# Optimization experiments

Measured on AMD Instinct MI355X. Metric: run time of the kernel, lower is better.

The kernel has to match this reference:

```python
import jax, jax.numpy as jnp
import numpy as np

EMBED_DIM = 2048
HIDDEN_DIM = 2048
SEQ_LEN = 8192


def setup_inputs() -> dict:
    key = jax.random.key(0)
    ks = jax.random.split(key, 6)
    x = jax.random.normal(ks[0], (SEQ_LEN, EMBED_DIM), dtype=jnp.float32)
    # original uses torch.rand (uniform [0,1)) for params
    W_h = jax.random.uniform(ks[1], (HIDDEN_DIM, HIDDEN_DIM), dtype=jnp.float32)
    W_x = jax.random.uniform(ks[2], (HIDDEN_DIM, EMBED_DIM), dtype=jnp.float32)
    W_y = jax.random.uniform(ks[3], (EMBED_DIM, HIDDEN_DIM), dtype=jnp.float32)
    B_h = jax.random.uniform(ks[4], (HIDDEN_DIM,), dtype=jnp.float32)
    B_y = jax.random.uniform(ks[5], (EMBED_DIM,), dtype=jnp.float32)
    return {"x": x, "W_h": W_h, "W_x": W_x, "W_y": W_y, "B_h": B_h, "B_y": B_y}


def reference(x, W_h, W_x, W_y, B_h, B_y):
    # Precompute input projections for all timesteps in one GEMM: [T, H]
    xp = x @ W_x.T + B_h

    def step(h, xp_t):
        h_new = jnp.tanh(W_h @ h + xp_t)  # [H]
        return h_new, h_new

    h0 = jnp.zeros((W_h.shape[0],), dtype=x.dtype)
    h_final, hs = jax.lax.scan(step, h0, xp)  # hs: [T, H]
    # Output projection + softmax over embed dim, batched over timesteps
    logits = hs @ W_y.T + B_y  # [T, E]
    output = jax.nn.softmax(logits, axis=-1)
    return (h_final, output)
```

## Files before the change

### kernel.cpp

```cpp
#include <hip/hip_runtime.h>

#define T_SEQ 8192
#define HDIM  2048
#define EDIM  2048
#define RBLK  64
#define ROWS_PER_BLK (HDIM / RBLK)

typedef unsigned long long u64;
typedef __attribute__((ext_vector_type(4))) unsigned int u32x4;
typedef __attribute__((ext_vector_type(4))) float f32x4;

__device__ inline void poll_pair(const u64* p0, const u64* p1, u32x4& a, u32x4& b) {
    asm volatile("global_load_dwordx4 %0, %2, off sc1\n\t"
                 "global_load_dwordx4 %1, %3, off sc1\n\t"
                 "s_waitcnt vmcnt(0)"
                 : "=v"(a), "=v"(b) : "v"(p0), "v"(p1) : "memory");
}

__device__ inline f32x4 ld_w16(const float* p) {
    f32x4 r;
    asm volatile("global_load_dwordx4 %0, %1, off" : "=v"(r) : "v"(p));
    return r;
}

__global__ __launch_bounds__(256) void gemm_nt_bias(
    const float* __restrict__ A, const float* __restrict__ B,
    const float* __restrict__ bias, float* __restrict__ C,
    int M, int N, int K)
{
    constexpr int BK = 32;
    __shared__ float As[BK][64 + 4];
    __shared__ float Bs[BK][64 + 4];

    const int tx = threadIdx.x & 15;
    const int ty = threadIdx.x >> 4;
    const int m0 = blockIdx.y * 64;
    const int n0 = blockIdx.x * 64;

    float acc[4][4] = {};

    for (int kk = 0; kk < K; kk += BK) {
        #pragma unroll
        for (int p = 0; p < 8; ++p) {
            int idx = p * 256 + threadIdx.x;
            int r = idx >> 5;
            int c = idx & 31;
            As[c][r] = A[(size_t)(m0 + r) * K + kk + c];
            Bs[c][r] = B[(size_t)(n0 + r) * K + kk + c];
        }
        __syncthreads();
        #pragma unroll
        for (int k = 0; k < BK; ++k) {
            float4 a = *(const float4*)&As[k][ty * 4];
            float4 b = *(const float4*)&Bs[k][tx * 4];
            float av[4] = {a.x, a.y, a.z, a.w};
            float bv[4] = {b.x, b.y, b.z, b.w};
            #pragma unroll
            for (int i = 0; i < 4; ++i)
                #pragma unroll
                for (int j = 0; j < 4; ++j)
                    acc[i][j] = fmaf(av[i], bv[j], acc[i][j]);
        }
        __syncthreads();
    }

    float4 bb = *(const float4*)&bias[n0 + tx * 4];
    float bvv[4] = {bb.x, bb.y, bb.z, bb.w};
    #pragma unroll
    for (int i = 0; i < 4; ++i) {
        float4 o;
        o.x = acc[i][0] + bvv[0];
        o.y = acc[i][1] + bvv[1];
        o.z = acc[i][2] + bvv[2];
        o.w = acc[i][3] + bvv[3];
        *(float4*)&C[(size_t)(m0 + ty * 4 + i) * N + n0 + tx * 4] = o;
    }
}

__global__ __launch_bounds__(512, 1) void rnn_recurrence(
    const float* __restrict__ Wh, const float* __restrict__ xp,
    float* __restrict__ Hs, u64* __restrict__ hbuf, int T)
{
    const int tid  = threadIdx.x;
    const int lane = tid & 63;
    const int wid  = tid >> 6;
    const int r0   = blockIdx.x * ROWS_PER_BLK + wid * 4;

    const float* wr0 = Wh + (size_t)(r0 + 0) * HDIM + lane * 4;
    const float* wr1 = Wh + (size_t)(r0 + 1) * HDIM + lane * 4;
    const float* wr2 = Wh + (size_t)(r0 + 2) * HDIM + lane * 4;
    const float* wr3 = Wh + (size_t)(r0 + 3) * HDIM + lane * 4;

    f32x4 w00 = ld_w16(wr0 + 0*256), w01 = ld_w16(wr0 + 1*256), w02 = ld_w16(wr0 + 2*256), w03 = ld_w16(wr0 + 3*256);
    f32x4 w04 = ld_w16(wr0 + 4*256), w05 = ld_w16(wr0 + 5*256), w06 = ld_w16(wr0 + 6*256), w07 = ld_w16(wr0 + 7*256);
    f32x4 w10 = ld_w16(wr1 + 0*256), w11 = ld_w16(wr1 + 1*256), w12 = ld_w16(wr1 + 2*256), w13 = ld_w16(wr1 + 3*256);
    f32x4 w14 = ld_w16(wr1 + 4*256), w15 = ld_w16(wr1 + 5*256), w16 = ld_w16(wr1 + 6*256), w17 = ld_w16(wr1 + 7*256);
    f32x4 w20 = ld_w16(wr2 + 0*256), w21 = ld_w16(wr2 + 1*256), w22 = ld_w16(wr2 + 2*256), w23 = ld_w16(wr2 + 3*256);
    f32x4 w24 = ld_w16(wr2 + 4*256), w25 = ld_w16(wr2 + 5*256), w26 = ld_w16(wr2 + 6*256), w27 = ld_w16(wr2 + 7*256);
    f32x4 w30 = ld_w16(wr3 + 0*256), w31 = ld_w16(wr3 + 1*256), w32 = ld_w16(wr3 + 2*256), w33 = ld_w16(wr3 + 3*256);
    f32x4 w34 = ld_w16(wr3 + 4*256), w35 = ld_w16(wr3 + 5*256), w36 = ld_w16(wr3 + 6*256), w37 = ld_w16(wr3 + 7*256);
    asm volatile("s_waitcnt vmcnt(0)" ::: "memory");

    __shared__ float hsm[HDIM];

    for (int t = 0; t < T; ++t) {
        float xq = 0.f;
        if (lane < 4) xq = xp[(size_t)t * HDIM + r0 + lane];

        float sv = 0.f;
        if (t > 0) {
            const u64* hb = hbuf + (size_t)(t & 1) * HDIM;
            const unsigned tg = (unsigned)t;
            const u64* p0 = hb + 2 * tid;
            const u64* p1 = hb + 1024 + 2 * tid;

            u32x4 a, b;
            poll_pair(p0, p1, a, b);
            while ((a.y != tg) | (a.w != tg) | (b.y != tg) | (b.w != tg))
                poll_pair(p0, p1, a, b);

            ((float2*)hsm)[tid] =
                make_float2(__uint_as_float(a.x), __uint_as_float(a.z));
            ((float2*)hsm)[tid + 512] =
                make_float2(__uint_as_float(b.x), __uint_as_float(b.z));
            __syncthreads();

            float s0 = 0.f, s1 = 0.f, s2 = 0.f, s3 = 0.f;
            #define RNN_STEP(IDX, WA, WB, WC, WD)                                   \
            {   float4 h4 = ((const float4*)hsm)[(IDX) * 64 + lane];                \
                s0 = fmaf(WA.x, h4.x, s0); s0 = fmaf(WA.y, h4.y, s0);               \
                s0 = fmaf(WA.z, h4.z, s0); s0 = fmaf(WA.w, h4.w, s0);               \
                s1 = fmaf(WB.x, h4.x, s1); s1 = fmaf(WB.y, h4.y, s1);               \
                s1 = fmaf(WB.z, h4.z, s1); s1 = fmaf(WB.w, h4.w, s1);               \
                s2 = fmaf(WC.x, h4.x, s2); s2 = fmaf(WC.y, h4.y, s2);               \
                s2 = fmaf(WC.z, h4.z, s2); s2 = fmaf(WC.w, h4.w, s2);               \
                s3 = fmaf(WD.x, h4.x, s3); s3 = fmaf(WD.y, h4.y, s3);               \
                s3 = fmaf(WD.z, h4.z, s3); s3 = fmaf(WD.w, h4.w, s3); }
            RNN_STEP(0, w00, w10, w20, w30)
            RNN_STEP(1, w01, w11, w21, w31)
            RNN_STEP(2, w02, w12, w22, w32)
            RNN_STEP(3, w03, w13, w23, w33)
            RNN_STEP(4, w04, w14, w24, w34)
            RNN_STEP(5, w05, w15, w25, w35)
            RNN_STEP(6, w06, w16, w26, w36)
            RNN_STEP(7, w07, w17, w27, w37)
            #undef RNN_STEP

            float fa = (lane & 1) ? s1 : s0;
            float fb = (lane & 1) ? s0 : s1;
            fa += __shfl_xor(fb, 1);
            float fc = (lane & 1) ? s3 : s2;
            float fd = (lane & 1) ? s2 : s3;
            fc += __shfl_xor(fd, 1);
            float fe = (lane & 2) ? fc : fa;
            float ff = (lane & 2) ? fa : fc;
            fe += __shfl_xor(ff, 2);
            #pragma unroll
            for (int off = 4; off < 64; off <<= 1) fe += __shfl_xor(fe, off);
            sv = fe;
        }

        if (lane < 4) {
            float hn = tanhf(sv + xq);
            u64 pk = ((u64)(unsigned)(t + 1) << 32) | (u64)__float_as_uint(hn);
            (void)__hip_atomic_exchange(
                &hbuf[(size_t)((t + 1) & 1) * HDIM + r0 + lane], pk,
                __ATOMIC_RELAXED, __HIP_MEMORY_SCOPE_AGENT);
            Hs[(size_t)t * HDIM + r0 + lane] = hn;
        }
    }
}

__global__ __launch_bounds__(256) void softmax_rows(
    const float* __restrict__ logits, float* __restrict__ out)
{
    const int row = blockIdx.x;
    const float4* in4 = (const float4*)(logits + (size_t)row * EDIM);
    float4* out4 = (float4*)(out + (size_t)row * EDIM);

    float4 v0 = in4[threadIdx.x];
    float4 v1 = in4[threadIdx.x + 256];

    float m = fmaxf(fmaxf(fmaxf(v0.x, v0.y), fmaxf(v0.z, v0.w)),
                    fmaxf(fmaxf(v1.x, v1.y), fmaxf(v1.z, v1.w)));
    #pragma unroll
    for (int off = 32; off > 0; off >>= 1) m = fmaxf(m, __shfl_xor(m, off));

    __shared__ float red[4];
    if ((threadIdx.x & 63) == 0) red[threadIdx.x >> 6] = m;
    __syncthreads();
    m = fmaxf(fmaxf(red[0], red[1]), fmaxf(red[2], red[3]));
    __syncthreads();

    float e[8];
    e[0] = expf(v0.x - m); e[1] = expf(v0.y - m);
    e[2] = expf(v0.z - m); e[3] = expf(v0.w - m);
    e[4] = expf(v1.x - m); e[5] = expf(v1.y - m);
    e[6] = expf(v1.z - m); e[7] = expf(v1.w - m);

    float s = e[0] + e[1] + e[2] + e[3] + e[4] + e[5] + e[6] + e[7];
    #pragma unroll
    for (int off = 32; off > 0; off >>= 1) s += __shfl_xor(s, off);
    if ((threadIdx.x & 63) == 0) red[threadIdx.x >> 6] = s;
    __syncthreads();
    s = red[0] + red[1] + red[2] + red[3];

    float inv = 1.0f / s;
    out4[threadIdx.x]       = make_float4(e[0] * inv, e[1] * inv, e[2] * inv, e[3] * inv);
    out4[threadIdx.x + 256] = make_float4(e[4] * inv, e[5] * inv, e[6] * inv, e[7] * inv);
}

__global__ void copy_vec(const float* __restrict__ src, float* __restrict__ dst, int n)
{
    int i = blockIdx.x * blockDim.x + threadIdx.x;
    if (i < n) dst[i] = src[i];
}

extern "C" void kernel_launch(void* const* d_in, const int* in_sizes, int n_in,
                              void* d_out, int out_size, void* d_ws, size_t ws_size,
                              hipStream_t stream)
{
    const float* x  = (const float*)d_in[0];
    const float* Wh = (const float*)d_in[1];
    const float* Wx = (const float*)d_in[2];
    const float* Wy = (const float*)d_in[3];
    const float* Bh = (const float*)d_in[4];
    const float* By = (const float*)d_in[5];

    float* out    = (float*)d_out;
    float* hfinal = out;
    float* hs     = out + HDIM;

    float* xp   = (float*)d_ws;
    u64*   hbuf = (u64*)((char*)d_ws + (size_t)T_SEQ * HDIM * 4);
    float* logits = xp;

    hipMemsetAsync(hbuf, 0, 2 * HDIM * sizeof(u64), stream);

    gemm_nt_bias<<<dim3(HDIM / 64, T_SEQ / 64), 256, 0, stream>>>(
        x, Wx, Bh, xp, T_SEQ, HDIM, EDIM);

    int T = T_SEQ;
    const float* xp_c = xp;
    void* args[] = {(void*)&Wh, (void*)&xp_c, (void*)&hs, (void*)&hbuf, (void*)&T};
    hipLaunchCooperativeKernel((void*)rnn_recurrence, dim3(RBLK), dim3(512),
                               args, 0, stream);

    gemm_nt_bias<<<dim3(EDIM / 64, T_SEQ / 64), 256, 0, stream>>>(
        hs, Wy, By, logits, T_SEQ, EDIM, HDIM);

    copy_vec<<<dim3(HDIM / 256), 256, 0, stream>>>(
        hs + (size_t)(T_SEQ - 1) * HDIM, hfinal, HDIM);

    softmax_rows<<<dim3(T_SEQ), 256, 0, stream>>>(logits, hs);
}
```

Before: 15.31 ms.

## Double-buffer polling loads and lighten barrier and publish in RNN recurrence

The spin-wait on the shared hidden-state buffer now keeps two pairs of loads in flight, waiting on vmcnt(2) so a fresh poll is already outstanding when a stale one is checked. This cuts the latency of seeing each step's data. The __syncthreads is replaced by an explicit lgkmcnt wait, s_barrier and sched_barrier, and the atomic exchange that publishes h is replaced by a relaxed atomic store. These target per-timestep synchronization latency in the latency-bound sequential scan. The extra in-flight loads add memory traffic, and the vmcnt accounting relies on no other outstanding loads, notably the xq load issued earlier.

```diff
diff --git a/kernel.cpp b/kernel.cpp
--- a/kernel.cpp
+++ b/kernel.cpp
@@ -10,11 +10,13 @@
 typedef __attribute__((ext_vector_type(4))) unsigned int u32x4;
 typedef __attribute__((ext_vector_type(4))) float f32x4;
 
-__device__ inline void poll_pair(const u64* p0, const u64* p1, u32x4& a, u32x4& b) {
+__device__ inline void issue2(const u64* p0, const u64* p1, u32x4& a, u32x4& b) {
     asm volatile("global_load_dwordx4 %0, %2, off sc1\n\t"
-                 "global_load_dwordx4 %1, %3, off sc1\n\t"
-                 "s_waitcnt vmcnt(0)"
+                 "global_load_dwordx4 %1, %3, off sc1"
                  : "=v"(a), "=v"(b) : "v"(p0), "v"(p1) : "memory");
+}
+__device__ inline void wait2(u32x4& x, u32x4& y) {
+    asm volatile("s_waitcnt vmcnt(2)" : "+v"(x), "+v"(y) :: "memory");
 }
 
 __device__ inline f32x4 ld_w16(const float* p) {
@@ -114,16 +116,32 @@
             const u64* p0 = hb + 2 * tid;
             const u64* p1 = hb + 1024 + 2 * tid;
 
-            u32x4 a, b;
-            poll_pair(p0, p1, a, b);
-            while ((a.y != tg) | (a.w != tg) | (b.y != tg) | (b.w != tg))
-                poll_pair(p0, p1, a, b);
+            u32x4 a0, b0, a1, b1;
+            issue2(p0, p1, a0, b0);
+            issue2(p0, p1, a1, b1);
+            bool use0 = true;
+            for (;;) {
+                wait2(a0, b0);
+                if ((a0.y == tg) & (a0.w == tg) & (b0.y == tg) & (b0.w == tg)) {
+                    use0 = true; break;
+                }
+                issue2(p0, p1, a0, b0);
+                wait2(a1, b1);
+                if ((a1.y == tg) & (a1.w == tg) & (b1.y == tg) & (b1.w == tg)) {
+                    use0 = false; break;
+                }
+                issue2(p0, p1, a1, b1);
+            }
+            u32x4 A = use0 ? a0 : a1;
+            u32x4 B = use0 ? b0 : b1;
 
             ((float2*)hsm)[tid] =
-                make_float2(__uint_as_float(a.x), __uint_as_float(a.z));
+                make_float2(__uint_as_float(A.x), __uint_as_float(A.z));
             ((float2*)hsm)[tid + 512] =
-                make_float2(__uint_as_float(b.x), __uint_as_float(b.z));
-            __syncthreads();
+                make_float2(__uint_as_float(B.x), __uint_as_float(B.z));
+            asm volatile("s_waitcnt lgkmcnt(0)" ::: "memory");
+            __builtin_amdgcn_s_barrier();
+            __builtin_amdgcn_sched_barrier(0);
 
             float s0 = 0.f, s1 = 0.f, s2 = 0.f, s3 = 0.f;
             #define RNN_STEP(IDX, WA, WB, WC, WD)                                   \
@@ -163,9 +181,8 @@
         if (lane < 4) {
             float hn = tanhf(sv + xq);
             u64 pk = ((u64)(unsigned)(t + 1) << 32) | (u64)__float_as_uint(hn);
-            (void)__hip_atomic_exchange(
-                &hbuf[(size_t)((t + 1) & 1) * HDIM + r0 + lane], pk,
-                __ATOMIC_RELAXED, __HIP_MEMORY_SCOPE_AGENT);
+            __hip_atomic_store(&hbuf[(size_t)((t + 1) & 1) * HDIM + r0 + lane], pk,
+                               __ATOMIC_RELAXED, __HIP_MEMORY_SCOPE_AGENT);
             Hs[(size_t)t * HDIM + r0 + lane] = hn;
         }
     }
```

After: 16.28 ms. +6.3%, slower.

## Store input projection transposed and use fast exp-based tanh in recurrence

Applied to the files above, without the earlier changes.

The input-projection GEMM now writes its result transposed, so each hidden row's timesteps sit next to each other in memory. The recurrence then reads xp for its 4 rows from locations that stay cache-friendly across consecutive steps. The libm tanhf on the serial critical path is replaced by a clamped v_exp_f32/v_rcp_f32 formulation to shorten per-step latency. The transposed store in the GEMM epilogue is strided by M, which may slow that GEMM, and the fast tanh is slightly less accurate.

```diff
diff --git a/kernel.cpp b/kernel.cpp
--- a/kernel.cpp
+++ b/kernel.cpp
@@ -21,6 +21,15 @@
     f32x4 r;
     asm volatile("global_load_dwordx4 %0, %1, off" : "=v"(r) : "v"(p));
     return r;
+}
+
+__device__ inline float fast_tanh(float z) {
+    float zc = fminf(fmaxf(z, -15.f), 15.f);
+    float zs = zc * 2.88539008177792681f;
+    float ez; asm("v_exp_f32 %0, %1" : "=v"(ez) : "v"(zs));
+    float rc; float ezp = ez + 1.f;
+    asm("v_rcp_f32 %0, %1" : "=v"(rc) : "v"(ezp));
+    return (ez - 1.f) * rc;
 }
 
 __global__ __launch_bounds__(256) void gemm_nt_bias(
@@ -77,8 +86,62 @@
     }
 }
 
+__global__ __launch_bounds__(256) void gemm_nt_bias_tc(
+    const float* __restrict__ A, const float* __restrict__ B,
+    const float* __restrict__ bias, float* __restrict__ Ct,
+    int M, int N, int K)
+{
+    constexpr int BK = 32;
+    __shared__ float As[BK][64 + 4];
+    __shared__ float Bs[BK][64 + 4];
+
+    const int tx = threadIdx.x & 15;
+    const int ty = threadIdx.x >> 4;
+    const int m0 = blockIdx.y * 64;
+    const int n0 = blockIdx.x * 64;
+
+    float acc[4][4] = {};
+
+    for (int kk = 0; kk < K; kk += BK) {
+        #pragma unroll
+        for (int p = 0; p < 8; ++p) {
+            int idx = p * 256 + threadIdx.x;
+            int r = idx >> 5;
+            int c = idx & 31;
+            As[c][r] = A[(size_t)(m0 + r) * K + kk + c];
+            Bs[c][r] = B[(size_t)(n0 + r) * K + kk + c];
+        }
+        __syncthreads();
+        #pragma unroll
+        for (int k = 0; k < BK; ++k) {
+            float4 a = *(const float4*)&As[k][ty * 4];
+            float4 b = *(const float4*)&Bs[k][tx * 4];
+            float av[4] = {a.x, a.y, a.z, a.w};
+            float bv[4] = {b.x, b.y, b.z, b.w};
+            #pragma unroll
+            for (int i = 0; i < 4; ++i)
+                #pragma unroll
+                for (int j = 0; j < 4; ++j)
+                    acc[i][j] = fmaf(av[i], bv[j], acc[i][j]);
+        }
+        __syncthreads();
+    }
+
+    float4 bb = *(const float4*)&bias[n0 + tx * 4];
+    float bvv[4] = {bb.x, bb.y, bb.z, bb.w};
+    #pragma unroll
+    for (int j = 0; j < 4; ++j) {
+        float4 o;
+        o.x = acc[0][j] + bvv[j];
+        o.y = acc[1][j] + bvv[j];
+        o.z = acc[2][j] + bvv[j];
+        o.w = acc[3][j] + bvv[j];
+        *(float4*)&Ct[(size_t)(n0 + tx * 4 + j) * M + m0 + ty * 4] = o;
+    }
+}
+
 __global__ __launch_bounds__(512, 1) void rnn_recurrence(
-    const float* __restrict__ Wh, const float* __restrict__ xp,
+    const float* __restrict__ Wh, const float* __restrict__ xpT,
     float* __restrict__ Hs, u64* __restrict__ hbuf, int T)
 {
     const int tid  = threadIdx.x;
@@ -105,7 +168,7 @@
 
     for (int t = 0; t < T; ++t) {
         float xq = 0.f;
-        if (lane < 4) xq = xp[(size_t)t * HDIM + r0 + lane];
+        if (lane < 4) xq = xpT[(size_t)(r0 + lane) * T + t];
 
         float sv = 0.f;
         if (t > 0) {
@@ -161,7 +224,7 @@
         }
 
         if (lane < 4) {
-            float hn = tanhf(sv + xq);
+            float hn = fast_tanh(sv + xq);
             u64 pk = ((u64)(unsigned)(t + 1) << 32) | (u64)__float_as_uint(hn);
             (void)__hip_atomic_exchange(
                 &hbuf[(size_t)((t + 1) & 1) * HDIM + r0 + lane], pk,
@@ -231,18 +294,18 @@
     float* hfinal = out;
     float* hs     = out + HDIM;
 
-    float* xp   = (float*)d_ws;
+    float* xpT  = (float*)d_ws;
     u64*   hbuf = (u64*)((char*)d_ws + (size_t)T_SEQ * HDIM * 4);
-    float* logits = xp;
+    float* logits = xpT;
 
     hipMemsetAsync(hbuf, 0, 2 * HDIM * sizeof(u64), stream);
 
-    gemm_nt_bias<<<dim3(HDIM / 64, T_SEQ / 64), 256, 0, stream>>>(
-        x, Wx, Bh, xp, T_SEQ, HDIM, EDIM);
+    gemm_nt_bias_tc<<<dim3(HDIM / 64, T_SEQ / 64), 256, 0, stream>>>(
+        x, Wx, Bh, xpT, T_SEQ, HDIM, EDIM);
 
     int T = T_SEQ;
-    const float* xp_c = xp;
-    void* args[] = {(void*)&Wh, (void*)&xp_c, (void*)&hs, (void*)&hbuf, (void*)&T};
+    const float* xpT_c = xpT;
+    void* args[] = {(void*)&Wh, (void*)&xpT_c, (void*)&hs, (void*)&hbuf, (void*)&T};
     hipLaunchCooperativeKernel((void*)rnn_recurrence, dim3(RBLK), dim3(512),
                                args, 0, stream);
 
```

Measured after the change: 14.82 ms. 3.2% less time.

## Fuse input GEMM, recurrence and output GEMM into one persistent cooperative kernel

Applied to the files above, without the earlier changes.

Launches a single cooperative kernel in which 64 blocks run the sequential recurrence while 192 worker blocks compute the input projection (written transposed) and, if workspace allows, the output projection. Counters and a progress flag let the recurrence start once the first xp tiles exist and let the output GEMM consume hidden states as they are published. This aims to hide both GEMMs behind the latency-bound recurrence, and it also swaps tanhf for an exp/rcp approximation. The risks are that worker blocks contend with the recurrence blocks for memory bandwidth and CUs, and that the spin-wait dependencies and occupancy assumptions could stall or deadlock.

```diff
diff --git a/kernel.cpp b/kernel.cpp
--- a/kernel.cpp
+++ b/kernel.cpp
@@ -4,11 +4,14 @@
 #define HDIM  2048
 #define EDIM  2048
 #define RBLK  64
+#define NWORK 192
 #define ROWS_PER_BLK (HDIM / RBLK)
 
 typedef unsigned long long u64;
+typedef unsigned int u32;
 typedef __attribute__((ext_vector_type(4))) unsigned int u32x4;
 typedef __attribute__((ext_vector_type(4))) float f32x4;
+typedef __attribute__((ext_vector_type(2))) float f32x2;
 
 __device__ inline void poll_pair(const u64* p0, const u64* p1, u32x4& a, u32x4& b) {
     asm volatile("global_load_dwordx4 %0, %2, off sc1\n\t"
@@ -16,11 +19,247 @@
                  "s_waitcnt vmcnt(0)"
                  : "=v"(a), "=v"(b) : "v"(p0), "v"(p1) : "memory");
 }
-
 __device__ inline f32x4 ld_w16(const float* p) {
     f32x4 r;
     asm volatile("global_load_dwordx4 %0, %1, off" : "=v"(r) : "v"(p));
     return r;
+}
+__device__ inline u32 ld_u32_sc1(const u32* p) {
+    u32 r;
+    asm volatile("global_load_dword %0, %1, off sc1\n\ts_waitcnt vmcnt(0)"
+                 : "=v"(r) : "v"(p) : "memory");
+    return r;
+}
+__device__ inline void st_u32_sc1(u32* p, u32 v) {
+    asm volatile("global_store_dword %0, %1, off sc1" :: "v"(p), "v"(v) : "memory");
+}
+__device__ inline void st8_sc1(float* p, f32x2 v) {
+    asm volatile("global_store_dwordx2 %0, %1, off sc1" :: "v"(p), "v"(v) : "memory");
+}
+
+__device__ inline float fast_tanh(float z) {
+    float zc = fminf(fmaxf(z, -15.f), 15.f);
+    float zs = zc * 2.88539008177792681f;
+    float ez; asm("v_exp_f32 %0, %1" : "=v"(ez) : "v"(zs));
+    float rc; float ezp = ez + 1.f;
+    asm("v_rcp_f32 %0, %1" : "=v"(rc) : "v"(ezp));
+    return (ez - 1.f) * rc;
+}
+
+__global__ __launch_bounds__(512, 2) void rnn_fused(
+    const float* __restrict__ x,  const float* __restrict__ Wh,
+    const float* __restrict__ Wx, const float* __restrict__ Wy,
+    const float* __restrict__ Bh, const float* __restrict__ By,
+    float* __restrict__ xpT, float* __restrict__ Hs, u64* __restrict__ hbuf,
+    u32* __restrict__ cnt, u32* __restrict__ pub, u32* __restrict__ done,
+    float* __restrict__ lbuf, int fuse3)
+{
+    __shared__ union {
+        float hsm[HDIM];
+        struct { float As[32][68]; float Bs[32][68]; } g;
+    } sm;
+
+    const int tid = threadIdx.x;
+
+    if (blockIdx.x < RBLK) {
+        const int lane = tid & 63;
+        const int wid  = tid >> 6;
+        const int r0   = blockIdx.x * ROWS_PER_BLK + wid * 4;
+
+        const float* wr0 = Wh + (size_t)(r0 + 0) * HDIM + lane * 4;
+        const float* wr1 = Wh + (size_t)(r0 + 1) * HDIM + lane * 4;
+        const float* wr2 = Wh + (size_t)(r0 + 2) * HDIM + lane * 4;
+        const float* wr3 = Wh + (size_t)(r0 + 3) * HDIM + lane * 4;
+
+        f32x4 w00 = ld_w16(wr0 + 0*256), w01 = ld_w16(wr0 + 1*256), w02 = ld_w16(wr0 + 2*256), w03 = ld_w16(wr0 + 3*256);
+        f32x4 w04 = ld_w16(wr0 + 4*256), w05 = ld_w16(wr0 + 5*256), w06 = ld_w16(wr0 + 6*256), w07 = ld_w16(wr0 + 7*256);
+        f32x4 w10 = ld_w16(wr1 + 0*256), w11 = ld_w16(wr1 + 1*256), w12 = ld_w16(wr1 + 2*256), w13 = ld_w16(wr1 + 3*256);
+        f32x4 w14 = ld_w16(wr1 + 4*256), w15 = ld_w16(wr1 + 5*256), w16 = ld_w16(wr1 + 6*256), w17 = ld_w16(wr1 + 7*256);
+        f32x4 w20 = ld_w16(wr2 + 0*256), w21 = ld_w16(wr2 + 1*256), w22 = ld_w16(wr2 + 2*256), w23 = ld_w16(wr2 + 3*256);
+        f32x4 w24 = ld_w16(wr2 + 4*256), w25 = ld_w16(wr2 + 5*256), w26 = ld_w16(wr2 + 6*256), w27 = ld_w16(wr2 + 7*256);
+        f32x4 w30 = ld_w16(wr3 + 0*256), w31 = ld_w16(wr3 + 1*256), w32 = ld_w16(wr3 + 2*256), w33 = ld_w16(wr3 + 3*256);
+        f32x4 w34 = ld_w16(wr3 + 4*256), w35 = ld_w16(wr3 + 5*256), w36 = ld_w16(wr3 + 6*256), w37 = ld_w16(wr3 + 7*256);
+        asm volatile("s_waitcnt vmcnt(0)" ::: "memory");
+
+        for (int t = 0; t < T_SEQ; ++t) {
+            if ((t & 63) == 0) {
+                const u32 c = (u32)(t >> 6);
+                while (ld_u32_sc1(&cnt[c]) != 32u) __builtin_amdgcn_s_sleep(8);
+            }
+            float xq = 0.f;
+            if (lane < 4) xq = xpT[(size_t)(r0 + lane) * T_SEQ + t];
+
+            float sv = 0.f;
+            if (t > 0) {
+                const u64* hb = hbuf + (size_t)(t & 1) * HDIM;
+                const unsigned tg = (unsigned)t;
+                const u64* p0 = hb + 2 * tid;
+                const u64* p1 = hb + 1024 + 2 * tid;
+
+                u32x4 a, b;
+                poll_pair(p0, p1, a, b);
+                while ((a.y != tg) | (a.w != tg) | (b.y != tg) | (b.w != tg))
+                    poll_pair(p0, p1, a, b);
+
+                if (blockIdx.x == 0 && tid == 0) st_u32_sc1(pub, (u32)t);
+
+                ((float2*)sm.hsm)[tid] =
+                    make_float2(__uint_as_float(a.x), __uint_as_float(a.z));
+                ((float2*)sm.hsm)[tid + 512] =
+                    make_float2(__uint_as_float(b.x), __uint_as_float(b.z));
+                __syncthreads();
+
+                float s0 = 0.f, s1 = 0.f, s2 = 0.f, s3 = 0.f;
+                #define RNN_STEP(IDX, WA, WB, WC, WD)                                   \
+                {   float4 h4 = ((const float4*)sm.hsm)[(IDX) * 64 + lane];             \
+                    s0 = fmaf(WA.x, h4.x, s0); s0 = fmaf(WA.y, h4.y, s0);               \
+                    s0 = fmaf(WA.z, h4.z, s0); s0 = fmaf(WA.w, h4.w, s0);               \
+                    s1 = fmaf(WB.x, h4.x, s1); s1 = fmaf(WB.y, h4.y, s1);               \
+                    s1 = fmaf(WB.z, h4.z, s1); s1 = fmaf(WB.w, h4.w, s1);               \
+                    s2 = fmaf(WC.x, h4.x, s2); s2 = fmaf(WC.y, h4.y, s2);               \
+                    s2 = fmaf(WC.z, h4.z, s2); s2 = fmaf(WC.w, h4.w, s2);               \
+                    s3 = fmaf(WD.x, h4.x, s3); s3 = fmaf(WD.y, h4.y, s3);               \
+                    s3 = fmaf(WD.z, h4.z, s3); s3 = fmaf(WD.w, h4.w, s3); }
+                RNN_STEP(0, w00, w10, w20, w30)
+                RNN_STEP(1, w01, w11, w21, w31)
+                RNN_STEP(2, w02, w12, w22, w32)
+                RNN_STEP(3, w03, w13, w23, w33)
+                RNN_STEP(4, w04, w14, w24, w34)
+                RNN_STEP(5, w05, w15, w25, w35)
+                RNN_STEP(6, w06, w16, w26, w36)
+                RNN_STEP(7, w07, w17, w27, w37)
+                #undef RNN_STEP
+
+                float fa = (lane & 1) ? s1 : s0;
+                float fb = (lane & 1) ? s0 : s1;
+                fa += __shfl_xor(fb, 1);
+                float fc = (lane & 1) ? s3 : s2;
+                float fd = (lane & 1) ? s2 : s3;
+                fc += __shfl_xor(fd, 1);
+                float fe = (lane & 2) ? fc : fa;
+                float ff = (lane & 2) ? fa : fc;
+                fe += __shfl_xor(ff, 2);
+                #pragma unroll
+                for (int off = 4; off < 64; off <<= 1) fe += __shfl_xor(fe, off);
+                sv = fe;
+            }
+
+            if (lane < 4) {
+                float hn = fast_tanh(sv + xq);
+                u64 pk = ((u64)(unsigned)(t + 1) << 32) | (u64)__float_as_uint(hn);
+                __hip_atomic_store(&hbuf[(size_t)((t + 1) & 1) * HDIM + r0 + lane], pk,
+                                   __ATOMIC_RELAXED, __HIP_MEMORY_SCOPE_AGENT);
+                __hip_atomic_store(&Hs[(size_t)t * HDIM + r0 + lane], hn,
+                                   __ATOMIC_RELAXED, __HIP_MEMORY_SCOPE_AGENT);
+            }
+        }
+        asm volatile("s_waitcnt vmcnt(0)" ::: "memory");
+        __syncthreads();
+        if (tid == 0) atomicAdd(done, 1u);
+
+    } else {
+        const int wblk = blockIdx.x - RBLK;
+        const int ty = tid >> 4, tx = tid & 15;
+        const int ty2 = ty * 2, tx4 = tx * 4;
+
+        for (int i = wblk; i < (T_SEQ / 64) * (HDIM / 64); i += NWORK) {
+            const int tcol = i >> 5;
+            const int nrow = i & 31;
+            if (tcol > 8) {
+                const u32 needp = (u32)((tcol - 8) * 64);
+                if (tid == 0)
+                    while (ld_u32_sc1(pub) < needp) __builtin_amdgcn_s_sleep(32);
+                __syncthreads();
+            }
+            const int m0 = tcol * 64, n0 = nrow * 64;
+
+            float a00 = 0.f, a01 = 0.f, a02 = 0.f, a03 = 0.f;
+            float a10 = 0.f, a11 = 0.f, a12 = 0.f, a13 = 0.f;
+            for (int kk = 0; kk < EDIM; kk += 32) {
+                #pragma unroll
+                for (int p = 0; p < 4; ++p) {
+                    int idx = p * 512 + tid;
+                    int r = idx >> 5, c = idx & 31;
+                    sm.g.As[c][r] = x [(size_t)(m0 + r) * EDIM + kk + c];
+                    sm.g.Bs[c][r] = Wx[(size_t)(n0 + r) * EDIM + kk + c];
+                }
+                __syncthreads();
+                #pragma unroll
+                for (int k = 0; k < 32; ++k) {
+                    const float q0 = sm.g.As[k][ty2], q1 = sm.g.As[k][ty2 + 1];
+                    const float4 b = *(const float4*)&sm.g.Bs[k][tx4];
+                    a00 = fmaf(q0, b.x, a00); a01 = fmaf(q0, b.y, a01);
+                    a02 = fmaf(q0, b.z, a02); a03 = fmaf(q0, b.w, a03);
+                    a10 = fmaf(q1, b.x, a10); a11 = fmaf(q1, b.y, a11);
+                    a12 = fmaf(q1, b.z, a12); a13 = fmaf(q1, b.w, a13);
+                }
+                __syncthreads();
+            }
+            {
+                float accr[2][4] = {{a00,a01,a02,a03},{a10,a11,a12,a13}};
+                #pragma unroll
+                for (int j = 0; j < 4; ++j) {
+                    float bb = Bh[n0 + tx4 + j];
+                    f32x2 v; v.x = accr[0][j] + bb; v.y = accr[1][j] + bb;
+                    st8_sc1(&xpT[(size_t)(n0 + tx4 + j) * T_SEQ + m0 + ty2], v);
+                }
+            }
+            asm volatile("s_waitcnt vmcnt(0)" ::: "memory");
+            __syncthreads();
+            if (tid == 0) atomicAdd(&cnt[tcol], 1u);
+        }
+
+        if (fuse3) {
+            for (int i = wblk; i < (T_SEQ / 64) * (EDIM / 64); i += NWORK) {
+                const int mrow = i >> 5, ncol = i & 31;
+                const int m0 = mrow * 64, n0 = ncol * 64;
+                const u32 needp = (u32)(m0 + 65);
+                if (tid == 0) {
+                    if (needp <= (u32)(T_SEQ - 1)) {
+                        while (ld_u32_sc1(pub) < needp) __builtin_amdgcn_s_sleep(32);
+                    } else {
+                        while (ld_u32_sc1(done) < (u32)RBLK) __builtin_amdgcn_s_sleep(32);
+                    }
+                }
+                __syncthreads();
+
+                float a00 = 0.f, a01 = 0.f, a02 = 0.f, a03 = 0.f;
+                float a10 = 0.f, a11 = 0.f, a12 = 0.f, a13 = 0.f;
+                for (int kk = 0; kk < HDIM; kk += 32) {
+                    #pragma unroll
+                    for (int p = 0; p < 4; ++p) {
+                        int idx = p * 512 + tid;
+                        int r = idx >> 5, c = idx & 31;
+                        sm.g.As[c][r] = Hs[(size_t)(m0 + r) * HDIM + kk + c];
+                        sm.g.Bs[c][r] = Wy[(size_t)(n0 + r) * HDIM + kk + c];
+                    }
+                    __syncthreads();
+                    #pragma unroll
+                    for (int k = 0; k < 32; ++k) {
+                        const float q0 = sm.g.As[k][ty2], q1 = sm.g.As[k][ty2 + 1];
+                        const float4 b = *(const float4*)&sm.g.Bs[k][tx4];
+                        a00 = fmaf(q0, b.x, a00); a01 = fmaf(q0, b.y, a01);
+                        a02 = fmaf(q0, b.z, a02); a03 = fmaf(q0, b.w, a03);
+                        a10 = fmaf(q1, b.x, a10); a11 = fmaf(q1, b.y, a11);
+                        a12 = fmaf(q1, b.z, a12); a13 = fmaf(q1, b.w, a13);
+                    }
+                    __syncthreads();
+                }
+                {
+                    float accr[2][4] = {{a00,a01,a02,a03},{a10,a11,a12,a13}};
+                    #pragma unroll
+                    for (int r = 0; r < 2; ++r) {
+                        float4 o;
+                        o.x = accr[r][0] + By[n0 + tx4 + 0];
+                        o.y = accr[r][1] + By[n0 + tx4 + 1];
+                        o.z = accr[r][2] + By[n0 + tx4 + 2];
+                        o.w = accr[r][3] + By[n0 + tx4 + 3];
+                        *(float4*)&lbuf[(size_t)(m0 + ty2 + r) * EDIM + n0 + tx4] = o;
+                    }
+                }
+            }
+        }
+    }
 }
 
 __global__ __launch_bounds__(256) void gemm_nt_bias(
@@ -38,13 +277,11 @@
     const int n0 = blockIdx.x * 64;
 
     float acc[4][4] = {};
-
     for (int kk = 0; kk < K; kk += BK) {
         #pragma unroll
         for (int p = 0; p < 8; ++p) {
             int idx = p * 256 + threadIdx.x;
-            int r = idx >> 5;
-            int c = idx & 31;
+            int r = idx >> 5, c = idx & 31;
             As[c][r] = A[(size_t)(m0 + r) * K + kk + c];
             Bs[c][r] = B[(size_t)(n0 + r) * K + kk + c];
         }
@@ -63,7 +300,6 @@
         }
         __syncthreads();
     }
-
     float4 bb = *(const float4*)&bias[n0 + tx * 4];
     float bvv[4] = {bb.x, bb.y, bb.z, bb.w};
     #pragma unroll
@@ -77,100 +313,6 @@
     }
 }
 
-__global__ __launch_bounds__(512, 1) void rnn_recurrence(
-    const float* __restrict__ Wh, const float* __restrict__ xp,
-    float* __restrict__ Hs, u64* __restrict__ hbuf, int T)
-{
-    const int tid  = threadIdx.x;
-    const int lane = tid & 63;
-    const int wid  = tid >> 6;
-    const int r0   = blockIdx.x * ROWS_PER_BLK + wid * 4;
-
-    const float* wr0 = Wh + (size_t)(r0 + 0) * HDIM + lane * 4;
-    const float* wr1 = Wh + (size_t)(r0 + 1) * HDIM + lane * 4;
-    const float* wr2 = Wh + (size_t)(r0 + 2) * HDIM + lane * 4;
-    const float* wr3 = Wh + (size_t)(r0 + 3) * HDIM + lane * 4;
-
-    f32x4 w00 = ld_w16(wr0 + 0*256), w01 = ld_w16(wr0 + 1*256), w02 = ld_w16(wr0 + 2*256), w03 = ld_w16(wr0 + 3*256);
-    f32x4 w04 = ld_w16(wr0 + 4*256), w05 = ld_w16(wr0 + 5*256), w06 = ld_w16(wr0 + 6*256), w07 = ld_w16(wr0 + 7*256);
-    f32x4 w10 = ld_w16(wr1 + 0*256), w11 = ld_w16(wr1 + 1*256), w12 = ld_w16(wr1 + 2*256), w13 = ld_w16(wr1 + 3*256);
-    f32x4 w14 = ld_w16(wr1 + 4*256), w15 = ld_w16(wr1 + 5*256), w16 = ld_w16(wr1 + 6*256), w17 = ld_w16(wr1 + 7*256);
-    f32x4 w20 = ld_w16(wr2 + 0*256), w21 = ld_w16(wr2 + 1*256), w22 = ld_w16(wr2 + 2*256), w23 = ld_w16(wr2 + 3*256);
-    f32x4 w24 = ld_w16(wr2 + 4*256), w25 = ld_w16(wr2 + 5*256), w26 = ld_w16(wr2 + 6*256), w27 = ld_w16(wr2 + 7*256);
-    f32x4 w30 = ld_w16(wr3 + 0*256), w31 = ld_w16(wr3 + 1*256), w32 = ld_w16(wr3 + 2*256), w33 = ld_w16(wr3 + 3*256);
-    f32x4 w34 = ld_w16(wr3 + 4*256), w35 = ld_w16(wr3 + 5*256), w36 = ld_w16(wr3 + 6*256), w37 = ld_w16(wr3 + 7*256);
-    asm volatile("s_waitcnt vmcnt(0)" ::: "memory");
-
-    __shared__ float hsm[HDIM];
-
-    for (int t = 0; t < T; ++t) {
-        float xq = 0.f;
-        if (lane < 4) xq = xp[(size_t)t * HDIM + r0 + lane];
-
-        float sv = 0.f;
-        if (t > 0) {
-            const u64* hb = hbuf + (size_t)(t & 1) * HDIM;
-            const unsigned tg = (unsigned)t;
-            const u64* p0 = hb + 2 * tid;
-            const u64* p1 = hb + 1024 + 2 * tid;
-
-            u32x4 a, b;
-            poll_pair(p0, p1, a, b);
-            while ((a.y != tg) | (a.w != tg) | (b.y != tg) | (b.w != tg))
-                poll_pair(p0, p1, a, b);
-
-            ((float2*)hsm)[tid] =
-                make_float2(__uint_as_float(a.x), __uint_as_float(a.z));
-            ((float2*)hsm)[tid + 512] =
-                make_float2(__uint_as_float(b.x), __uint_as_float(b.z));
-            __syncthreads();
-
-            float s0 = 0.f, s1 = 0.f, s2 = 0.f, s3 = 0.f;
-            #define RNN_STEP(IDX, WA, WB, WC, WD)                                   \
-            {   float4 h4 = ((const float4*)hsm)[(IDX) * 64 + lane];                \
-                s0 = fmaf(WA.x, h4.x, s0); s0 = fmaf(WA.y, h4.y, s0);               \
-                s0 = fmaf(WA.z, h4.z, s0); s0 = fmaf(WA.w, h4.w, s0);               \
-                s1 = fmaf(WB.x, h4.x, s1); s1 = fmaf(WB.y, h4.y, s1);               \
-                s1 = fmaf(WB.z, h4.z, s1); s1 = fmaf(WB.w, h4.w, s1);               \
-                s2 = fmaf(WC.x, h4.x, s2); s2 = fmaf(WC.y, h4.y, s2);               \
-                s2 = fmaf(WC.z, h4.z, s2); s2 = fmaf(WC.w, h4.w, s2);               \
-                s3 = fmaf(WD.x, h4.x, s3); s3 = fmaf(WD.y, h4.y, s3);               \
-                s3 = fmaf(WD.z, h4.z, s3); s3 = fmaf(WD.w, h4.w, s3); }
-            RNN_STEP(0, w00, w10, w20, w30)
-            RNN_STEP(1, w01, w11, w21, w31)
-            RNN_STEP(2, w02, w12, w22, w32)
-            RNN_STEP(3, w03, w13, w23, w33)
-            RNN_STEP(4, w04, w14, w24, w34)
-            RNN_STEP(5, w05, w15, w25, w35)
-            RNN_STEP(6, w06, w16, w26, w36)
-            RNN_STEP(7, w07, w17, w27, w37)
-            #undef RNN_STEP
-
-            float fa = (lane & 1) ? s1 : s0;
-            float fb = (lane & 1) ? s0 : s1;
-            fa += __shfl_xor(fb, 1);
-            float fc = (lane & 1) ? s3 : s2;
-            float fd = (lane & 1) ? s2 : s3;
-            fc += __shfl_xor(fd, 1);
-            float fe = (lane & 2) ? fc : fa;
-            float ff = (lane & 2) ? fa : fc;
-            fe += __shfl_xor(ff, 2);
-            #pragma unroll
-            for (int off = 4; off < 64; off <<= 1) fe += __shfl_xor(fe, off);
-            sv = fe;
-        }
-
-        if (lane < 4) {
-            float hn = tanhf(sv + xq);
-            u64 pk = ((u64)(unsigned)(t + 1) << 32) | (u64)__float_as_uint(hn);
-            (void)__hip_atomic_exchange(
-                &hbuf[(size_t)((t + 1) & 1) * HDIM + r0 + lane], pk,
-                __ATOMIC_RELAXED, __HIP_MEMORY_SCOPE_AGENT);
-            Hs[(size_t)t * HDIM + r0 + lane] = hn;
-        }
-    }
-}
-
 __global__ __launch_bounds__(256) void softmax_rows(
     const float* __restrict__ logits, float* __restrict__ out)
 {
@@ -231,23 +373,35 @@
     float* hfinal = out;
     float* hs     = out + HDIM;
 
-    float* xp   = (float*)d_ws;
-    u64*   hbuf = (u64*)((char*)d_ws + (size_t)T_SEQ * HDIM * 4);
-    float* logits = xp;
-
-    hipMemsetAsync(hbuf, 0, 2 * HDIM * sizeof(u64), stream);
-
-    gemm_nt_bias<<<dim3(HDIM / 64, T_SEQ / 64), 256, 0, stream>>>(
-        x, Wx, Bh, xp, T_SEQ, HDIM, EDIM);
-
-    int T = T_SEQ;
-    const float* xp_c = xp;
-    void* args[] = {(void*)&Wh, (void*)&xp_c, (void*)&hs, (void*)&hbuf, (void*)&T};
-    hipLaunchCooperativeKernel((void*)rnn_recurrence, dim3(RBLK), dim3(512),
+    char*  base = (char*)d_ws;
+    float* xpT  = (float*)base;
+    u64*   hbuf = (u64*)(base + (size_t)T_SEQ * HDIM * 4);
+    u32*   cnt  = (u32*)((char*)hbuf + 2 * HDIM * sizeof(u64));
+    u32*   pub  = cnt + 128;
+    u32*   done = pub + 1;
+    float* lbuf = (float*)(base + (size_t)T_SEQ * HDIM * 4 + 65536);
+
+    size_t need_fuse3 = (size_t)T_SEQ * HDIM * 4 * 2 + 65536 + (size_t)T_SEQ * EDIM * 4 - (size_t)T_SEQ * HDIM * 4;
+    need_fuse3 = (size_t)T_SEQ * HDIM * 4 + 65536 + (size_t)T_SEQ * EDIM * 4;
+    int fuse3 = (ws_size >= need_fuse3) ? 1 : 0;
+
+    hipMemsetAsync(hbuf, 0, 2 * HDIM * sizeof(u64) + 1024, stream);
+
+    const float* x_c = x; const float* Wh_c = Wh; const float* Wx_c = Wx;
+    const float* Wy_c = Wy; const float* Bh_c = Bh; const float* By_c = By;
+    void* args[] = {(void*)&x_c, (void*)&Wh_c, (void*)&Wx_c, (void*)&Wy_c,
+                    (void*)&Bh_c, (void*)&By_c,
+                    (void*)&xpT, (void*)&hs, (void*)&hbuf,
+                    (void*)&cnt, (void*)&pub, (void*)&done,
+                    (void*)&lbuf, (void*)&fuse3};
+    hipLaunchCooperativeKernel((void*)rnn_fused, dim3(RBLK + NWORK), dim3(512),
                                args, 0, stream);
 
-    gemm_nt_bias<<<dim3(EDIM / 64, T_SEQ / 64), 256, 0, stream>>>(
-        hs, Wy, By, logits, T_SEQ, EDIM, HDIM);
+    float* logits = fuse3 ? lbuf : xpT;
+    if (!fuse3) {
+        gemm_nt_bias<<<dim3(EDIM / 64, T_SEQ / 64), 256, 0, stream>>>(
+            hs, Wy, By, logits, T_SEQ, EDIM, HDIM);
+    }
 
     copy_vec<<<dim3(HDIM / 256), 256, 0, stream>>>(
         hs + (size_t)(T_SEQ - 1) * HDIM, hfinal, HDIM);
```

Measured after the change: 22.46 ms. 46.7% more time.
